# Kernel tuning notes

Measured on AMD Instinct MI355X. Metric: run time of the kernel, lower is better.

The kernel has to match this reference:

```python
import jax, jax.numpy as jnp
import numpy as np
from jax import lax

NUM_SPLIT = 16
DCT = 7
# top16 frequency indices (first 16 of the top lists)
MAPPER_X = np.array([0, 0, 6, 0, 0, 1, 1, 4, 5, 1, 3, 0, 0, 0, 3, 2], dtype=np.int32)
MAPPER_Y = np.array([0, 1, 0, 5, 2, 0, 2, 0, 0, 6, 0, 4, 6, 3, 5, 2], dtype=np.int32)


def _dct_table():
    pos = np.arange(DCT)
    freq = np.arange(DCT)[:, None]
    d = np.cos(np.pi * freq * (pos + 0.5) / DCT) / np.sqrt(DCT)
    d[1:] *= np.sqrt(2.0)
    return d.astype(np.float32)  # (7, 7): [freq, pos]


def _gconv(x, w, b, groups):
    y = lax.conv_general_dilated(x, w, (2, 2), 'VALID',
                                 dimension_numbers=('NCHW', 'OIHW', 'NCHW'),
                                 feature_group_count=groups)
    return y + b[None, :, None, None]


def setup_inputs() -> dict:
    key = jax.random.key(0)
    ks = jax.random.split(key, 7)
    n, c, h, w = 32, 512, 56, 56
    r = 16
    return {
        'x': jax.random.normal(ks[0], (n, c, h, w), jnp.float32),
        'conv1_w': jax.random.normal(ks[1], (NUM_SPLIT, c // NUM_SPLIT, 3, 3), jnp.float32) * 0.05,
        'conv1_b': jax.random.normal(ks[2], (NUM_SPLIT,), jnp.float32) * 0.05,
        'conv2_w': jax.random.normal(ks[3], (NUM_SPLIT, 1, 3, 3), jnp.float32) * 0.3,
        'conv2_b': jax.random.normal(ks[4], (NUM_SPLIT,), jnp.float32) * 0.3,
        'w1': jax.random.normal(ks[5], (c // r, c), jnp.float32) * 0.05,
        'w2': jax.random.normal(ks[6], (c, c // r), jnp.float32) * 0.2,
    }


def reference(x, conv1_w, conv1_b, conv2_w, conv2_b, w1, w2):
    n, c, h, w = x.shape
    c_part = c // NUM_SPLIT
    D = jnp.asarray(_dct_table(), x.dtype)
    mx = jnp.asarray(MAPPER_X)
    my = jnp.asarray(MAPPER_Y)

    # adaptive_avg_pool2d to 7x7 (h,w divisible by 7 -> exact block mean)
    xp = x.reshape(n, c, DCT, h // DCT, DCT, w // DCT).mean(axis=(3, 5))

    # filters_predicted: grouped conv 7x7 -> 3x3 -> 1x1
    a1 = jax.nn.hard_sigmoid(_gconv(xp, conv1_w, conv1_b, NUM_SPLIT))
    v = _gconv(a1, conv2_w, conv2_b, NUM_SPLIT).reshape(n, NUM_SPLIT)
    # adaptive_avg_pool1d(1 -> 16) repeats v; matmul with ones(16,1) sums -> v * 16
    pred = jnp.clip(v * NUM_SPLIT, 0.0, NUM_SPLIT - 1.1)

    left = pred.astype(jnp.int32)   # (n, 16)
    frac = pred - left
    right = left + 1

    def dct_weights(idx):  # idx (n,16) -> per-split 7x7 DCT filters (n,16,7,7)
        fx = D[mx[idx]]  # (n,16,7)
        fy = D[my[idx]]
        return fx[..., :, None] * fy[..., None, :]

    xp_s = xp.reshape(n, NUM_SPLIT, c_part, DCT, DCT)
    res_l = jnp.einsum('nskhw,nshw->nsk', xp_s, dct_weights(left)) * (1.0 - frac)[:, :, None]
    res_r = jnp.einsum('nskhw,nshw->nsk', xp_s, dct_weights(right)) * frac[:, :, None]
    s = (res_l + res_r).reshape(n, c)

    hmid = jax.nn.hard_sigmoid(s @ w1.T)
    cw = jax.nn.sigmoid(hmid @ w2.T)  # (n, c)
    return x * cw[:, :, None, None]
```

## Files before the change

### kernel.cpp

```cpp
#include <hip/hip_runtime.h>

#define N_   32
#define C_   512
#define H_   56
#define W_   56
#define S_   16
#define CP_  32
#define HW_  (H_*W_)
#define TOT_ ((size_t)N_*C_*HW_)

typedef float f32x4 __attribute__((ext_vector_type(4)));

__constant__ int d_mx[16] = {0,0,6,0,0,1,1,4,5,1,3,0,0,0,3,2};
__constant__ int d_my[16] = {0,1,0,5,2,0,2,0,0,6,0,4,6,3,5,2};

__global__ void __launch_bounds__(256) pool_kernel(const float* __restrict__ x,
                                                   float* __restrict__ xp) {
    __shared__ float tile[HW_];
    __shared__ float part[49 * 4];
    int plane = blockIdx.x;
    int t = threadIdx.x;
    const float4* src = reinterpret_cast<const float4*>(x + (size_t)plane * HW_);
    for (int i = t; i < HW_ / 4; i += 256)
        *reinterpret_cast<float4*>(&tile[i * 4]) = src[i];
    __syncthreads();
    if (t < 196) {
        int bin = t >> 2, q = t & 3;
        int oi = bin / 7, oj = bin % 7;
        const float* rp = &tile[(oi * 8 + q * 2) * W_ + oj * 8];
        float s = 0.f;
#pragma unroll
        for (int rr = 0; rr < 2; ++rr)
#pragma unroll
            for (int cc = 0; cc < 8; ++cc) s += rp[rr * W_ + cc];
        part[t] = s;
    }
    __syncthreads();
    if (t < 49) {
        float s = part[t * 4] + part[t * 4 + 1] + part[t * 4 + 2] + part[t * 4 + 3];
        xp[(size_t)plane * 49 + t] = s * (1.0f / 64.0f);
    }
}

__global__ void __launch_bounds__(256) head_kernel(
        const float* __restrict__ xp,
        const float* __restrict__ c1w, const float* __restrict__ c1b,
        const float* __restrict__ c2w, const float* __restrict__ c2b,
        const float* __restrict__ w1,  const float* __restrict__ w2,
        float* __restrict__ cwout) {
    __shared__ float tile[C_ * 49];
    __shared__ float sD[7][7];
    __shared__ float a1[S_ * 9];
    __shared__ float wcomb[S_ * 49];
    __shared__ float svec[C_];
    __shared__ float hpart[256];
    __shared__ float hmid[32];
    __shared__ float sfrac[S_];
    __shared__ int   sleft[S_];

    int n = blockIdx.x, t = threadIdx.x;
    const float4* src = reinterpret_cast<const float4*>(xp + (size_t)n * C_ * 49);
    for (int i = t; i < C_ * 49 / 4; i += 256)
        *reinterpret_cast<float4*>(&tile[i * 4]) = src[i];

    if (t < 49) {
        int f = t / 7, p = t % 7;
        float v = cosf(3.14159265358979323846f * f * (p + 0.5f) / 7.0f) * 0.3779644730092272f;
        if (f >= 1) v *= 1.4142135623730951f;
        sD[f][p] = v;
    }
    __syncthreads();

    if (t < S_ * 9) {
        int s = t / 9, o = t - s * 9, oi = o / 3, oj = o - oi * 3;
        float acc = c1b[s];
        const float* xb = &tile[s * CP_ * 49];
        const float* wb = c1w + s * CP_ * 9;
        for (int ic = 0; ic < CP_; ++ic) {
#pragma unroll
            for (int ki = 0; ki < 3; ++ki)
#pragma unroll
                for (int kj = 0; kj < 3; ++kj)
                    acc += xb[ic * 49 + (oi * 2 + ki) * 7 + (oj * 2 + kj)]
                         * wb[ic * 9 + ki * 3 + kj];
        }
        a1[t] = fminf(fmaxf(acc + 3.f, 0.f), 6.f) * (1.f / 6.f);
    }
    __syncthreads();

    if (t < S_) {
        float acc = c2b[t];
#pragma unroll
        for (int k = 0; k < 9; ++k) acc += a1[t * 9 + k] * c2w[t * 9 + k];
        float pred = fminf(fmaxf(acc * 16.f, 0.f), 14.9f);
        int l = (int)pred;
        sleft[t] = l;
        sfrac[t] = pred - (float)l;
    }
    __syncthreads();

    for (int i = t; i < S_ * 49; i += 256) {
        int s = i / 49, p = i - s * 49, hh = p / 7, ww = p - hh * 7;
        int l = sleft[s], r = l + 1;
        float fr = sfrac[s];
        wcomb[i] = (1.f - fr) * sD[d_mx[l]][hh] * sD[d_my[l]][ww]
                 +        fr  * sD[d_mx[r]][hh] * sD[d_my[r]][ww];
    }
    __syncthreads();

    for (int ch = t; ch < C_; ch += 256) {
        const float* xb = &tile[ch * 49];
        const float* wb = &wcomb[(ch >> 5) * 49];
        float acc = 0.f;
#pragma unroll
        for (int p = 0; p < 49; ++p) acc += xb[p] * wb[p];
        svec[ch] = acc;
    }
    __syncthreads();

    {
        int o = t >> 3, g = t & 7;
        const float4* wv = reinterpret_cast<const float4*>(w1 + o * C_ + g * 64);
        const float4* sv = reinterpret_cast<const float4*>(&svec[g * 64]);
        float acc = 0.f;
#pragma unroll
        for (int j = 0; j < 16; ++j) {
            float4 a = sv[j], b = wv[j];
            acc += a.x * b.x + a.y * b.y + a.z * b.z + a.w * b.w;
        }
        hpart[t] = acc;
    }
    __syncthreads();
    if (t < 32) {
        float acc = 0.f;
#pragma unroll
        for (int g = 0; g < 8; ++g) acc += hpart[t * 8 + g];
        hmid[t] = fminf(fmaxf(acc + 3.f, 0.f), 6.f) * (1.f / 6.f);
    }
    __syncthreads();

    for (int ch = t; ch < C_; ch += 256) {
        const float4* wr = reinterpret_cast<const float4*>(w2 + ch * 32);
        float acc = 0.f;
#pragma unroll
        for (int j = 0; j < 8; ++j) {
            float4 b = wr[j];
            const float4 h = reinterpret_cast<const float4*>(hmid)[j];
            acc += h.x * b.x + h.y * b.y + h.z * b.z + h.w * b.w;
        }
        cwout[n * C_ + ch] = 1.f / (1.f + expf(-acc));
    }
}

__global__ void __launch_bounds__(256) scale_kernel(const float* __restrict__ x,
                                                    const float* __restrict__ cw,
                                                    float* __restrict__ out) {
    int plane = blockIdx.x;
    int t = threadIdx.x;
    float wsc = cw[plane];
    const f32x4* src = reinterpret_cast<const f32x4*>(x + (size_t)plane * HW_);
    f32x4* dst = reinterpret_cast<f32x4*>(out + (size_t)plane * HW_);

    f32x4 u0 = src[t];
    f32x4 u1 = src[t + 256];
    f32x4 u2 = src[t + 512];
    f32x4 u3;
    if (t < 16) u3 = src[t + 768];

    u0 *= wsc;
    u1 *= wsc;
    u2 *= wsc;

    __builtin_nontemporal_store(u0, dst + t);
    __builtin_nontemporal_store(u1, dst + t + 256);
    __builtin_nontemporal_store(u2, dst + t + 512);
    if (t < 16) {
        u3 *= wsc;
        __builtin_nontemporal_store(u3, dst + t + 768);
    }
}

extern "C" void kernel_launch(void* const* d_in, const int* in_sizes, int n_in,
                              void* d_out, int out_size, void* d_ws, size_t ws_size,
                              hipStream_t stream) {
    const float* x   = (const float*)d_in[0];
    const float* c1w = (const float*)d_in[1];
    const float* c1b = (const float*)d_in[2];
    const float* c2w = (const float*)d_in[3];
    const float* c2b = (const float*)d_in[4];
    const float* w1  = (const float*)d_in[5];
    const float* w2  = (const float*)d_in[6];
    float* out = (float*)d_out;

    float* xp    = (float*)d_ws;
    float* cwbuf = xp + (size_t)N_ * C_ * 49;

    pool_kernel<<<N_ * C_, 256, 0, stream>>>(x, xp);
    head_kernel<<<N_, 256, 0, stream>>>(xp, c1w, c1b, c2w, c2b, w1, w2, cwbuf);
    scale_kernel<<<N_ * C_, 256, 0, stream>>>(x, cwbuf, out);
}
```

Baseline: 394.4 us.

## Fuse pool, head and scale into one cooperative persistent kernel

Replaces the three launches with a single cooperative kernel of 1024 blocks that uses grid-wide syncs between phases: pooling, per-(n,split) DCT head, the FC1 layer, then the sigmoid scale pass. The head work is spread across 512 blocks instead of 32, which removes the serial single-block-per-sample bottleneck and two kernel launch gaps. The costs are three grid barriers and a second full read of x that happens long after the first, so it may miss in cache. It also relies on all 1024 blocks being co-resident.

```diff
diff --git a/kernel.cpp b/kernel.cpp
--- a/kernel.cpp
+++ b/kernel.cpp
@@ -1,4 +1,7 @@
 #include <hip/hip_runtime.h>
+#include <hip/hip_cooperative_groups.h>
+
+namespace cg = cooperative_groups;
 
 #define N_   32
 #define C_   512
@@ -7,176 +10,181 @@
 #define S_   16
 #define CP_  32
 #define HW_  (H_*W_)
-#define TOT_ ((size_t)N_*C_*HW_)
+#define PLANES_ (N_*C_)
+#define GRID_  1024
+#define PPB_   (PLANES_/GRID_)
+#define XPS_   64
 
 typedef float f32x4 __attribute__((ext_vector_type(4)));
 
 __constant__ int d_mx[16] = {0,0,6,0,0,1,1,4,5,1,3,0,0,0,3,2};
 __constant__ int d_my[16] = {0,1,0,5,2,0,2,0,0,6,0,4,6,3,5,2};
 
-__global__ void __launch_bounds__(256) pool_kernel(const float* __restrict__ x,
-                                                   float* __restrict__ xp) {
-    __shared__ float tile[HW_];
-    __shared__ float part[49 * 4];
-    int plane = blockIdx.x;
-    int t = threadIdx.x;
-    const float4* src = reinterpret_cast<const float4*>(x + (size_t)plane * HW_);
-    for (int i = t; i < HW_ / 4; i += 256)
-        *reinterpret_cast<float4*>(&tile[i * 4]) = src[i];
-    __syncthreads();
-    if (t < 196) {
-        int bin = t >> 2, q = t & 3;
-        int oi = bin / 7, oj = bin % 7;
-        const float* rp = &tile[(oi * 8 + q * 2) * W_ + oj * 8];
-        float s = 0.f;
-#pragma unroll
-        for (int rr = 0; rr < 2; ++rr)
-#pragma unroll
-            for (int cc = 0; cc < 8; ++cc) s += rp[rr * W_ + cc];
-        part[t] = s;
-    }
-    __syncthreads();
-    if (t < 49) {
-        float s = part[t * 4] + part[t * 4 + 1] + part[t * 4 + 2] + part[t * 4 + 3];
-        xp[(size_t)plane * 49 + t] = s * (1.0f / 64.0f);
-    }
-}
-
-__global__ void __launch_bounds__(256) head_kernel(
-        const float* __restrict__ xp,
+__global__ void __launch_bounds__(256, 4) fused_kernel(
+        const float* __restrict__ x,
         const float* __restrict__ c1w, const float* __restrict__ c1b,
         const float* __restrict__ c2w, const float* __restrict__ c2b,
         const float* __restrict__ w1,  const float* __restrict__ w2,
-        float* __restrict__ cwout) {
-    __shared__ float tile[C_ * 49];
-    __shared__ float sD[7][7];
-    __shared__ float a1[S_ * 9];
-    __shared__ float wcomb[S_ * 49];
-    __shared__ float svec[C_];
-    __shared__ float hpart[256];
-    __shared__ float hmid[32];
-    __shared__ float sfrac[S_];
-    __shared__ int   sleft[S_];
-
-    int n = blockIdx.x, t = threadIdx.x;
-    const float4* src = reinterpret_cast<const float4*>(xp + (size_t)n * C_ * 49);
-    for (int i = t; i < C_ * 49 / 4; i += 256)
-        *reinterpret_cast<float4*>(&tile[i * 4]) = src[i];
-
-    if (t < 49) {
-        int f = t / 7, p = t % 7;
-        float v = cosf(3.14159265358979323846f * f * (p + 0.5f) / 7.0f) * 0.3779644730092272f;
-        if (f >= 1) v *= 1.4142135623730951f;
-        sD[f][p] = v;
+        float* __restrict__ out,
+        float* __restrict__ xp,
+        float* __restrict__ svec_g,
+        float* __restrict__ hmid_g) {
+    __shared__ float tile[HW_];
+    __shared__ float part[196];
+    __shared__ float sD[49];
+    __shared__ float wcomb[49];
+    __shared__ float aux[64];
+    cg::grid_group grid = cg::this_grid();
+    const int bid = blockIdx.x, t = threadIdx.x;
+
+    for (int k = 0; k < PPB_; ++k) {
+        const int plane = bid + k * GRID_;
+        const f32x4* src = reinterpret_cast<const f32x4*>(x + (size_t)plane * HW_);
+        f32x4* tl = reinterpret_cast<f32x4*>(tile);
+        f32x4 u0 = src[t];
+        f32x4 u1 = src[t + 256];
+        f32x4 u2 = src[t + 512];
+        if (t < 16) tl[t + 768] = src[t + 768];
+        tl[t] = u0; tl[t + 256] = u1; tl[t + 512] = u2;
+        __syncthreads();
+        if (t < 196) {
+            int bin = t >> 2, q = t & 3;
+            int oi = bin / 7, oj = bin % 7;
+            const float* rp = &tile[(oi * 8 + q * 2) * W_ + oj * 8];
+            float s = 0.f;
+#pragma unroll
+            for (int rr = 0; rr < 2; ++rr)
+#pragma unroll
+                for (int cc = 0; cc < 8; ++cc) s += rp[rr * W_ + cc];
+            part[t] = s;
+        }
+        __syncthreads();
+        if (t < 49) {
+            float s = part[t * 4] + part[t * 4 + 1] + part[t * 4 + 2] + part[t * 4 + 3];
+            xp[(size_t)plane * XPS_ + t] = s * (1.0f / 64.0f);
+        }
+    }
+    __threadfence();
+    grid.sync();
+
+    if (bid < N_ * S_) {
+        const int n = bid >> 4, s = bid & 15;
+        const float* xs = xp + (size_t)(n * C_ + s * CP_) * XPS_;
+        for (int i = t; i < CP_ * 49; i += 256) {
+            int ch = i / 49, p = i - ch * 49;
+            tile[i] = xs[ch * XPS_ + p];
+        }
+        if (t < 49) {
+            int f = t / 7, p = t % 7;
+            float v = cosf(3.14159265358979323846f * f * (p + 0.5f) / 7.0f) * 0.3779644730092272f;
+            if (f >= 1) v *= 1.4142135623730951f;
+            sD[t] = v;
+        }
+        __syncthreads();
+        if (t < 9) {
+            int oi = t / 3, oj = t - oi * 3;
+            float acc = c1b[s];
+            const float* wb = c1w + s * CP_ * 9;
+            for (int ic = 0; ic < CP_; ++ic) {
+#pragma unroll
+                for (int ki = 0; ki < 3; ++ki)
+#pragma unroll
+                    for (int kj = 0; kj < 3; ++kj)
+                        acc += tile[ic * 49 + (oi * 2 + ki) * 7 + (oj * 2 + kj)]
+                             * wb[ic * 9 + ki * 3 + kj];
+            }
+            aux[t] = fminf(fmaxf(acc + 3.f, 0.f), 6.f) * (1.f / 6.f);
+        }
+        __syncthreads();
+        if (t == 0) {
+            float acc = c2b[s];
+#pragma unroll
+            for (int k = 0; k < 9; ++k) acc += aux[k] * c2w[s * 9 + k];
+            float pred = fminf(fmaxf(acc * 16.f, 0.f), 14.9f);
+            int l = (int)pred;
+            aux[16] = (float)l;
+            aux[17] = pred - (float)l;
+        }
+        __syncthreads();
+        if (t < 49) {
+            int hh = t / 7, ww = t - hh * 7;
+            int l = (int)aux[16], r = l + 1;
+            float fr = aux[17];
+            wcomb[t] = (1.f - fr) * sD[d_mx[l] * 7 + hh] * sD[d_my[l] * 7 + ww]
+                     +        fr  * sD[d_mx[r] * 7 + hh] * sD[d_my[r] * 7 + ww];
+        }
+        __syncthreads();
+        if (t < CP_) {
+            float acc = 0.f;
+#pragma unroll
+            for (int p = 0; p < 49; ++p) acc += tile[t * 49 + p] * wcomb[p];
+            svec_g[n * C_ + s * CP_ + t] = acc;
+        }
+    }
+    __threadfence();
+    grid.sync();
+
+    if (bid < N_) {
+        const int n = bid;
+        const f32x4* sv_g = reinterpret_cast<const f32x4*>(svec_g + n * C_);
+        f32x4* tl = reinterpret_cast<f32x4*>(tile);
+        for (int i = t; i < C_ / 4; i += 256) tl[i] = sv_g[i];
+        __syncthreads();
+        {
+            int o = t >> 3, g = t & 7;
+            const f32x4* wv = reinterpret_cast<const f32x4*>(w1 + o * C_ + g * 64);
+            const f32x4* sv = reinterpret_cast<const f32x4*>(tile + g * 64);
+            float acc = 0.f;
+#pragma unroll
+            for (int j = 0; j < 16; ++j) {
+                f32x4 a = sv[j], b = wv[j];
+                acc += a.x * b.x + a.y * b.y + a.z * b.z + a.w * b.w;
+            }
+            tile[512 + t] = acc;
+        }
+        __syncthreads();
+        if (t < 32) {
+            float acc = 0.f;
+#pragma unroll
+            for (int g = 0; g < 8; ++g) acc += tile[512 + t * 8 + g];
+            hmid_g[n * 32 + t] = fminf(fmaxf(acc + 3.f, 0.f), 6.f) * (1.f / 6.f);
+        }
+    }
+    __threadfence();
+    grid.sync();
+
+    if (t < PPB_) {
+        const int plane = bid + t * GRID_;
+        const int n = plane >> 9, c = plane & (C_ - 1);
+        const f32x4* hv = reinterpret_cast<const f32x4*>(hmid_g + n * 32);
+        const f32x4* wr = reinterpret_cast<const f32x4*>(w2 + c * 32);
+        float acc = 0.f;
+#pragma unroll
+        for (int j = 0; j < 8; ++j) {
+            f32x4 h = hv[j], b = wr[j];
+            acc += h.x * b.x + h.y * b.y + h.z * b.z + h.w * b.w;
+        }
+        aux[t] = 1.f / (1.f + expf(-acc));
     }
     __syncthreads();
-
-    if (t < S_ * 9) {
-        int s = t / 9, o = t - s * 9, oi = o / 3, oj = o - oi * 3;
-        float acc = c1b[s];
-        const float* xb = &tile[s * CP_ * 49];
-        const float* wb = c1w + s * CP_ * 9;
-        for (int ic = 0; ic < CP_; ++ic) {
-#pragma unroll
-            for (int ki = 0; ki < 3; ++ki)
-#pragma unroll
-                for (int kj = 0; kj < 3; ++kj)
-                    acc += xb[ic * 49 + (oi * 2 + ki) * 7 + (oj * 2 + kj)]
-                         * wb[ic * 9 + ki * 3 + kj];
-        }
-        a1[t] = fminf(fmaxf(acc + 3.f, 0.f), 6.f) * (1.f / 6.f);
-    }
-    __syncthreads();
-
-    if (t < S_) {
-        float acc = c2b[t];
-#pragma unroll
-        for (int k = 0; k < 9; ++k) acc += a1[t * 9 + k] * c2w[t * 9 + k];
-        float pred = fminf(fmaxf(acc * 16.f, 0.f), 14.9f);
-        int l = (int)pred;
-        sleft[t] = l;
-        sfrac[t] = pred - (float)l;
-    }
-    __syncthreads();
-
-    for (int i = t; i < S_ * 49; i += 256) {
-        int s = i / 49, p = i - s * 49, hh = p / 7, ww = p - hh * 7;
-        int l = sleft[s], r = l + 1;
-        float fr = sfrac[s];
-        wcomb[i] = (1.f - fr) * sD[d_mx[l]][hh] * sD[d_my[l]][ww]
-                 +        fr  * sD[d_mx[r]][hh] * sD[d_my[r]][ww];
-    }
-    __syncthreads();
-
-    for (int ch = t; ch < C_; ch += 256) {
-        const float* xb = &tile[ch * 49];
-        const float* wb = &wcomb[(ch >> 5) * 49];
-        float acc = 0.f;
-#pragma unroll
-        for (int p = 0; p < 49; ++p) acc += xb[p] * wb[p];
-        svec[ch] = acc;
-    }
-    __syncthreads();
-
-    {
-        int o = t >> 3, g = t & 7;
-        const float4* wv = reinterpret_cast<const float4*>(w1 + o * C_ + g * 64);
-        const float4* sv = reinterpret_cast<const float4*>(&svec[g * 64]);
-        float acc = 0.f;
-#pragma unroll
-        for (int j = 0; j < 16; ++j) {
-            float4 a = sv[j], b = wv[j];
-            acc += a.x * b.x + a.y * b.y + a.z * b.z + a.w * b.w;
-        }
-        hpart[t] = acc;
-    }
-    __syncthreads();
-    if (t < 32) {
-        float acc = 0.f;
-#pragma unroll
-        for (int g = 0; g < 8; ++g) acc += hpart[t * 8 + g];
-        hmid[t] = fminf(fmaxf(acc + 3.f, 0.f), 6.f) * (1.f / 6.f);
-    }
-    __syncthreads();
-
-    for (int ch = t; ch < C_; ch += 256) {
-        const float4* wr = reinterpret_cast<const float4*>(w2 + ch * 32);
-        float acc = 0.f;
-#pragma unroll
-        for (int j = 0; j < 8; ++j) {
-            float4 b = wr[j];
-            const float4 h = reinterpret_cast<const float4*>(hmid)[j];
-            acc += h.x * b.x + h.y * b.y + h.z * b.z + h.w * b.w;
-        }
-        cwout[n * C_ + ch] = 1.f / (1.f + expf(-acc));
-    }
-}
-
-__global__ void __launch_bounds__(256) scale_kernel(const float* __restrict__ x,
-                                                    const float* __restrict__ cw,
-                                                    float* __restrict__ out) {
-    int plane = blockIdx.x;
-    int t = threadIdx.x;
-    float wsc = cw[plane];
-    const f32x4* src = reinterpret_cast<const f32x4*>(x + (size_t)plane * HW_);
-    f32x4* dst = reinterpret_cast<f32x4*>(out + (size_t)plane * HW_);
-
-    f32x4 u0 = src[t];
-    f32x4 u1 = src[t + 256];
-    f32x4 u2 = src[t + 512];
-    f32x4 u3;
-    if (t < 16) u3 = src[t + 768];
-
-    u0 *= wsc;
-    u1 *= wsc;
-    u2 *= wsc;
-
-    __builtin_nontemporal_store(u0, dst + t);
-    __builtin_nontemporal_store(u1, dst + t + 256);
-    __builtin_nontemporal_store(u2, dst + t + 512);
-    if (t < 16) {
-        u3 *= wsc;
-        __builtin_nontemporal_store(u3, dst + t + 768);
+    for (int k = 0; k < PPB_; ++k) {
+        const int plane = bid + k * GRID_;
+        const float wsc = aux[k];
+        const f32x4* src = reinterpret_cast<const f32x4*>(x + (size_t)plane * HW_);
+        f32x4* dst = reinterpret_cast<f32x4*>(out + (size_t)plane * HW_);
+        f32x4 u0 = src[t];
+        f32x4 u1 = src[t + 256];
+        f32x4 u2 = src[t + 512];
+        f32x4 u3;
+        if (t < 16) u3 = src[t + 768];
+        u0 *= wsc; u1 *= wsc; u2 *= wsc;
+        __builtin_nontemporal_store(u0, dst + t);
+        __builtin_nontemporal_store(u1, dst + t + 256);
+        __builtin_nontemporal_store(u2, dst + t + 512);
+        if (t < 16) {
+            u3 *= wsc;
+            __builtin_nontemporal_store(u3, dst + t + 768);
+        }
     }
 }
 
@@ -192,10 +200,13 @@
     const float* w2  = (const float*)d_in[6];
     float* out = (float*)d_out;
 
-    float* xp    = (float*)d_ws;
-    float* cwbuf = xp + (size_t)N_ * C_ * 49;
-
-    pool_kernel<<<N_ * C_, 256, 0, stream>>>(x, xp);
-    head_kernel<<<N_, 256, 0, stream>>>(xp, c1w, c1b, c2w, c2b, w1, w2, cwbuf);
-    scale_kernel<<<N_ * C_, 256, 0, stream>>>(x, cwbuf, out);
+    float* xp   = (float*)d_ws;
+    float* svec = xp + (size_t)PLANES_ * XPS_;
+    float* hmid = svec + (size_t)N_ * C_;
+
+    void* args[] = { (void*)&x, (void*)&c1w, (void*)&c1b, (void*)&c2w, (void*)&c2b,
+                     (void*)&w1, (void*)&w2, (void*)&out, (void*)&xp, (void*)&svec,
+                     (void*)&hmid };
+    hipLaunchCooperativeKernel(reinterpret_cast<void*>(fused_kernel),
+                               dim3(GRID_), dim3(256), args, 0, stream);
 }
```

New measurement: 953.6 us. 142% more time.

## Fuse head computation into scale kernel with redundant per-block head recompute

Applied to the files above, without the earlier changes.

Merges the head kernel (conv, DCT weights, MLP) and the scale kernel into one kernel launched with 2048 blocks. Each block redoes the whole per-sample head from global xp, computes sigmoid weights for its 8 channels, then scales those 8 planes. The aim is to remove the serial 32-block head launch, which underuses the GPU, and one launch gap. In exchange the head work is repeated 64 times per sample, reading xp straight from global/L2 instead of a shared tile, and each block now does a serial head phase before streaming.

```diff
diff --git a/kernel.cpp b/kernel.cpp
--- a/kernel.cpp
+++ b/kernel.cpp
@@ -42,39 +42,38 @@
     }
 }
 
-__global__ void __launch_bounds__(256) head_kernel(
+__global__ void __launch_bounds__(256, 4) hs_kernel(
+        const float* __restrict__ x,
         const float* __restrict__ xp,
         const float* __restrict__ c1w, const float* __restrict__ c1b,
         const float* __restrict__ c2w, const float* __restrict__ c2b,
         const float* __restrict__ w1,  const float* __restrict__ w2,
-        float* __restrict__ cwout) {
-    __shared__ float tile[C_ * 49];
-    __shared__ float sD[7][7];
+        float* __restrict__ out) {
+    __shared__ float sD[49];
     __shared__ float a1[S_ * 9];
     __shared__ float wcomb[S_ * 49];
     __shared__ float svec[C_];
     __shared__ float hpart[256];
     __shared__ float hmid[32];
+    __shared__ float cwv[8];
     __shared__ float sfrac[S_];
     __shared__ int   sleft[S_];
 
-    int n = blockIdx.x, t = threadIdx.x;
-    const float4* src = reinterpret_cast<const float4*>(xp + (size_t)n * C_ * 49);
-    for (int i = t; i < C_ * 49 / 4; i += 256)
-        *reinterpret_cast<float4*>(&tile[i * 4]) = src[i];
+    const int bid = blockIdx.x, t = threadIdx.x;
+    const int n = bid >> 6;
+    const int r = bid & 63;
+    const float* xpn = xp + (size_t)n * C_ * 49;
 
-    if (t < 49) {
-        int f = t / 7, p = t % 7;
+    if (t >= 192 && t < 241) {
+        int u = t - 192, f = u / 7, p = u - f * 7;
         float v = cosf(3.14159265358979323846f * f * (p + 0.5f) / 7.0f) * 0.3779644730092272f;
         if (f >= 1) v *= 1.4142135623730951f;
-        sD[f][p] = v;
+        sD[u] = v;
     }
-    __syncthreads();
-
     if (t < S_ * 9) {
         int s = t / 9, o = t - s * 9, oi = o / 3, oj = o - oi * 3;
         float acc = c1b[s];
-        const float* xb = &tile[s * CP_ * 49];
+        const float* xb = xpn + s * CP_ * 49;
         const float* wb = c1w + s * CP_ * 9;
         for (int ic = 0; ic < CP_; ++ic) {
 #pragma unroll
@@ -101,15 +100,17 @@
 
     for (int i = t; i < S_ * 49; i += 256) {
         int s = i / 49, p = i - s * 49, hh = p / 7, ww = p - hh * 7;
-        int l = sleft[s], r = l + 1;
+        int l = sleft[s], rr = l + 1;
         float fr = sfrac[s];
-        wcomb[i] = (1.f - fr) * sD[d_mx[l]][hh] * sD[d_my[l]][ww]
-                 +        fr  * sD[d_mx[r]][hh] * sD[d_my[r]][ww];
+        wcomb[i] = (1.f - fr) * sD[d_mx[l] * 7 + hh] * sD[d_my[l] * 7 + ww]
+                 +        fr  * sD[d_mx[rr] * 7 + hh] * sD[d_my[rr] * 7 + ww];
     }
     __syncthreads();
 
-    for (int ch = t; ch < C_; ch += 256) {
-        const float* xb = &tile[ch * 49];
+#pragma unroll
+    for (int q = 0; q < 2; ++q) {
+        int ch = t + q * 256;
+        const float* xb = xpn + ch * 49;
         const float* wb = &wcomb[(ch >> 5) * 49];
         float acc = 0.f;
 #pragma unroll
@@ -120,12 +121,12 @@
 
     {
         int o = t >> 3, g = t & 7;
-        const float4* wv = reinterpret_cast<const float4*>(w1 + o * C_ + g * 64);
-        const float4* sv = reinterpret_cast<const float4*>(&svec[g * 64]);
+        const f32x4* wv = reinterpret_cast<const f32x4*>(w1 + o * C_ + g * 64);
+        const f32x4* sv = reinterpret_cast<const f32x4*>(&svec[g * 64]);
         float acc = 0.f;
 #pragma unroll
         for (int j = 0; j < 16; ++j) {
-            float4 a = sv[j], b = wv[j];
+            f32x4 a = sv[j], b = wv[j];
             acc += a.x * b.x + a.y * b.y + a.z * b.z + a.w * b.w;
         }
         hpart[t] = acc;
@@ -139,44 +140,39 @@
     }
     __syncthreads();
 
-    for (int ch = t; ch < C_; ch += 256) {
-        const float4* wr = reinterpret_cast<const float4*>(w2 + ch * 32);
+    if (t < 8) {
+        int c = r * 8 + t;
+        const f32x4* hv = reinterpret_cast<const f32x4*>(hmid);
+        const f32x4* wr = reinterpret_cast<const f32x4*>(w2 + c * 32);
         float acc = 0.f;
 #pragma unroll
         for (int j = 0; j < 8; ++j) {
-            float4 b = wr[j];
-            const float4 h = reinterpret_cast<const float4*>(hmid)[j];
+            f32x4 h = hv[j], b = wr[j];
             acc += h.x * b.x + h.y * b.y + h.z * b.z + h.w * b.w;
         }
-        cwout[n * C_ + ch] = 1.f / (1.f + expf(-acc));
+        cwv[t] = 1.f / (1.f + expf(-acc));
     }
-}
+    __syncthreads();
 
-__global__ void __launch_bounds__(256) scale_kernel(const float* __restrict__ x,
-                                                    const float* __restrict__ cw,
-                                                    float* __restrict__ out) {
-    int plane = blockIdx.x;
-    int t = threadIdx.x;
-    float wsc = cw[plane];
-    const f32x4* src = reinterpret_cast<const f32x4*>(x + (size_t)plane * HW_);
-    f32x4* dst = reinterpret_cast<f32x4*>(out + (size_t)plane * HW_);
-
-    f32x4 u0 = src[t];
-    f32x4 u1 = src[t + 256];
-    f32x4 u2 = src[t + 512];
-    f32x4 u3;
-    if (t < 16) u3 = src[t + 768];
-
-    u0 *= wsc;
-    u1 *= wsc;
-    u2 *= wsc;
-
-    __builtin_nontemporal_store(u0, dst + t);
-    __builtin_nontemporal_store(u1, dst + t + 256);
-    __builtin_nontemporal_store(u2, dst + t + 512);
-    if (t < 16) {
-        u3 *= wsc;
-        __builtin_nontemporal_store(u3, dst + t + 768);
+#pragma unroll 1
+    for (int k = 0; k < 8; ++k) {
+        const int plane = n * C_ + r * 8 + k;
+        const float wsc = cwv[k];
+        const f32x4* src = reinterpret_cast<const f32x4*>(x + (size_t)plane * HW_);
+        f32x4* dst = reinterpret_cast<f32x4*>(out + (size_t)plane * HW_);
+        f32x4 u0 = src[t];
+        f32x4 u1 = src[t + 256];
+        f32x4 u2 = src[t + 512];
+        f32x4 u3;
+        if (t < 16) u3 = src[t + 768];
+        u0 *= wsc; u1 *= wsc; u2 *= wsc;
+        __builtin_nontemporal_store(u0, dst + t);
+        __builtin_nontemporal_store(u1, dst + t + 256);
+        __builtin_nontemporal_store(u2, dst + t + 512);
+        if (t < 16) {
+            u3 *= wsc;
+            __builtin_nontemporal_store(u3, dst + t + 768);
+        }
     }
 }
 
@@ -192,10 +188,8 @@
     const float* w2  = (const float*)d_in[6];
     float* out = (float*)d_out;
 
-    float* xp    = (float*)d_ws;
-    float* cwbuf = xp + (size_t)N_ * C_ * 49;
+    float* xp = (float*)d_ws;
 
     pool_kernel<<<N_ * C_, 256, 0, stream>>>(x, xp);
-    head_kernel<<<N_, 256, 0, stream>>>(xp, c1w, c1b, c2w, c2b, w1, w2, cwbuf);
-    scale_kernel<<<N_ * C_, 256, 0, stream>>>(x, cwbuf, out);
+    hs_kernel<<<N_ * S_ * 4, 256, 0, stream>>>(x, xp, c1w, c1b, c2w, c2b, w1, w2, out);
 }
```

Result: slower. 430.9 us (+9.3%).
